# Kernel tuning notes

Measured on AMD Instinct MI355X. Metric: run time of the kernel, lower is better.

The kernel has to match this reference:

```python
import jax, jax.numpy as jnp
import numpy as np

BS, NA = 32, 128
NE = NA * (NA - 1)            # fully-connected directed, no self loops
NU, D = 4, 8                  # num_user, per-user feature dim
FEAT = NU * D                 # 32: node / edge feature dim
CC = 8                        # conv1 out channels (1x1 conv, in_channels=2)
CONV_OUT = CC * NU * D        # 256
EMB = 64                      # embedding size (x_last / output dim)
H1 = 256                      # MLP hidden
MLP1_IN = CONV_OUT + EMB      # layer_idx > 1: concat local_state_j
MLP2_IN = FEAT + EMB + EMB    # x0, x_last, agg_in


def make_edges():
    src, dst = np.meshgrid(np.arange(NA), np.arange(NA), indexing='ij')
    m = src != dst
    return jnp.asarray(np.stack([src[m], dst[m]], axis=1), dtype=jnp.int32)


def setup_inputs() -> dict:
    key = jax.random.key(0)
    ks = jax.random.split(key, 9)
    return {
        "x0": jax.random.normal(ks[0], (BS, NA, FEAT), jnp.float32),
        "x_last": jax.random.normal(ks[1], (BS, NA, EMB), jnp.float32),
        "edge_attr": jax.random.normal(ks[2], (BS, NE, FEAT), jnp.float32),
        "conv_w": jax.random.normal(ks[3], (CC, 2), jnp.float32) * 0.3,
        "conv_b": jnp.zeros((CC,), jnp.float32),
        "mlp1_w1": jax.random.normal(ks[4], (MLP1_IN, H1), jnp.float32) * 0.05,
        "mlp1_b1": jnp.zeros((H1,), jnp.float32),
        "mlp1_w2": jax.random.normal(ks[5], (H1, EMB), jnp.float32) * 0.05,
        "mlp1_b2": jnp.zeros((EMB,), jnp.float32),
        "mlp2_w1": jax.random.normal(ks[6], (MLP2_IN, H1), jnp.float32) * 0.05,
        "mlp2_b1": jnp.zeros((H1,), jnp.float32),
        "mlp2_w2": jax.random.normal(ks[7], (H1, EMB), jnp.float32) * 0.05,
        "mlp2_b2": jnp.zeros((EMB,), jnp.float32),
        "edge_idx": make_edges(),
    }


def reference(x0, x_last, edge_attr, conv_w, conv_b,
              mlp1_w1, mlp1_b1, mlp1_w2, mlp1_b2,
              mlp2_w1, mlp2_b1, mlp2_w2, mlp2_b2, edge_idx):
    src, dst = edge_idx[:, 0], edge_idx[:, 1]
    # --- propagate / local_embedding ---
    nf_j = x0[:, src, :]                 # [B, E, FEAT] gather source node feats
    ls_j = x_last[:, src, :]             # [B, E, EMB]  (layer_idx > 1)
    # torch: cat(node_feat, edge_attr) on user dim then view [N,2,NU,D]
    x = jnp.stack([nf_j.reshape(BS, NE, NU, D),
                   edge_attr.reshape(BS, NE, NU, D)], axis=2)  # [B,E,2,NU,D]
    # 1x1 Conv2d(2 -> CC) + ReLU
    y = jax.nn.relu(jnp.einsum('becud,oc->beoud', x, conv_w)
                    + conv_b[None, None, :, None, None])
    y = y.reshape(BS, NE, CONV_OUT)
    lf = jnp.concatenate([y, ls_j], axis=-1)                   # [B,E,MLP1_IN]
    h = jax.nn.relu(lf @ mlp1_w1 + mlp1_b1)
    local_embed = h @ mlp1_w2 + mlp1_b2                        # [B,E,EMB]
    # per-node segment sum over destination (replaces python loop over agents)
    agg_in = jnp.zeros((BS, NA, EMB), local_embed.dtype).at[:, dst, :].add(local_embed)
    # --- update_embedding ---
    agg = jnp.concatenate([x0, x_last, agg_in], axis=-1)       # [B,NA,MLP2_IN]
    h2 = jax.nn.relu(agg @ mlp2_w1 + mlp2_b1)
    return h2 @ mlp2_w2 + mlp2_b2                              # [B,NA,EMB]
```

## Files before the change

kernel.cpp:

```cpp
#include <hip/hip_runtime.h>
#include <hip/hip_bf16.h>

#define BSg   32
#define NAg   128
#define NEg   16256
#define EMBg  64
#define H1g   256

typedef __attribute__((ext_vector_type(8))) short  short8;
typedef __attribute__((ext_vector_type(4))) float  f32x4;

__device__ __forceinline__ unsigned short f2bf16u(float x) {
    union { __hip_bfloat16 h; unsigned short u; } cv;
    cv.h = __float2bfloat16(x);
    return cv.u;
}
__device__ __forceinline__ unsigned int pack2(float a, float b) {
    union { __hip_bfloat162 h; unsigned int u; } cv;
    cv.h = __float22bfloat162_rn(make_float2(a, b));
    return cv.u;
}

__global__ void pack_weights(const float* __restrict__ w1, unsigned short* __restrict__ w1p)
{
    int i = blockIdx.x * 256 + threadIdx.x;
    if (i < 320 * 256) {
        int k = i >> 8, n = i & 255;
        w1p[(k >> 3) * (256 * 8) + n * 8 + (k & 7)] = f2bf16u(w1[i]);
    }
}

__global__ __launch_bounds__(256, 4) void edge_kernel(
    const float* __restrict__ x0, const float* __restrict__ x_last,
    const float* __restrict__ edge_attr, const float* __restrict__ conv_w,
    const float* __restrict__ conv_b, const unsigned short* __restrict__ w1p,
    const float* __restrict__ b1, const float* __restrict__ w2f,
    const float* __restrict__ b2, float* __restrict__ agg)
{
    __shared__ unsigned short fragA[10 * 4 * 64 * 8];

    const int wgid = (blockIdx.x & 7) * 1024 + (blockIdx.x >> 3);
    const int half = wgid & 1;
    const int bd   = wgid >> 1;
    const int b    = bd >> 7, d = bd & 127;

    const int tid  = threadIdx.x;
    const int wq   = tid >> 6, lane = tid & 63;
    const int llo  = lane & 15, lhi = lane >> 4;
    const int colbase = wq * 64;

    short8 bf0[4];
    #pragma unroll
    for (int n = 0; n < 4; ++n)
        bf0[n] = *(const short8*)&w1p[(lhi * H1g + colbase + n * 16 + llo) * 8];

    {
        const int j  = wq * 16 + llo;
        const int el = half * 64 + j;
        int s = el + (el >= d ? 1 : 0);
        if (s > 127) s = 127;
        int e = s * 127 + d - (s < d ? 1 : 0);
        if (e > NEg - 1) e = NEg - 1;

        const float4* nfp = (const float4*)(x0        + (((size_t)b * NAg + s) << 5) + (lhi << 3));
        const float4* eap = (const float4*)(edge_attr + (((size_t)b * NEg + e) << 5) + (lhi << 3));
        float4 nf0 = nfp[0], nf1 = nfp[1];
        float4 ea0 = eap[0], ea1 = eap[1];

        #pragma unroll
        for (int o = 0; o < 8; ++o) {
            const float w0 = conv_w[2 * o], w1v = conv_w[2 * o + 1], cb = conv_b[o];
            float y0 = fmaxf(fmaf(w0, nf0.x, fmaf(w1v, ea0.x, cb)), 0.f);
            float y1 = fmaxf(fmaf(w0, nf0.y, fmaf(w1v, ea0.y, cb)), 0.f);
            float y2 = fmaxf(fmaf(w0, nf0.z, fmaf(w1v, ea0.z, cb)), 0.f);
            float y3 = fmaxf(fmaf(w0, nf0.w, fmaf(w1v, ea0.w, cb)), 0.f);
            float y4 = fmaxf(fmaf(w0, nf1.x, fmaf(w1v, ea1.x, cb)), 0.f);
            float y5 = fmaxf(fmaf(w0, nf1.y, fmaf(w1v, ea1.y, cb)), 0.f);
            float y6 = fmaxf(fmaf(w0, nf1.z, fmaf(w1v, ea1.z, cb)), 0.f);
            float y7 = fmaxf(fmaf(w0, nf1.w, fmaf(w1v, ea1.w, cb)), 0.f);
            uint4 pk;
            pk.x = pack2(y0, y1); pk.y = pack2(y2, y3);
            pk.z = pack2(y4, y5); pk.w = pack2(y6, y7);
            *(uint4*)&fragA[(((o * 4 + wq) * 64) + lane) * 8] = pk;
        }
        {
            const float4* lsp = (const float4*)(x_last + (((size_t)b * NAg + s) << 6) + (lhi << 4));
            float4 l0 = lsp[0], l1 = lsp[1], l2 = lsp[2], l3 = lsp[3];
            uint4 pa, pb;
            pa.x = pack2(l0.x, l0.y); pa.y = pack2(l0.z, l0.w);
            pa.z = pack2(l1.x, l1.y); pa.w = pack2(l1.z, l1.w);
            pb.x = pack2(l2.x, l2.y); pb.y = pack2(l2.z, l2.w);
            pb.z = pack2(l3.x, l3.y); pb.w = pack2(l3.z, l3.w);
            const int ks8  = 8 + (lhi >> 1);
            const int slot = (ks8 * 4 + wq) * 64 + ((lhi & 1) * 2) * 16 + llo;
            *(uint4*)&fragA[slot * 8]        = pa;
            *(uint4*)&fragA[(slot + 16) * 8] = pb;
        }
    }
    __syncthreads();

    f32x4 acc[4][4];
    #pragma unroll
    for (int m = 0; m < 4; ++m)
        #pragma unroll
        for (int n = 0; n < 4; ++n)
            acc[m][n] = (f32x4){0.f, 0.f, 0.f, 0.f};

    #pragma unroll
    for (int ks = 0; ks < 10; ++ks) {
        short8 af[4], bf[4];
        #pragma unroll
        for (int m = 0; m < 4; ++m)
            af[m] = *(const short8*)&fragA[((ks * 4 + m) * 64 + lane) * 8];
        #pragma unroll
        for (int n = 0; n < 4; ++n) {
            if (ks == 0) bf[n] = bf0[n];
            else         bf[n] = *(const short8*)&w1p[((ks * 4 + lhi) * H1g + colbase + n * 16 + llo) * 8];
        }
        #pragma unroll
        for (int m = 0; m < 4; ++m)
            #pragma unroll
            for (int n = 0; n < 4; ++n)
                acc[m][n] = __builtin_amdgcn_mfma_f32_16x16x32_bf16(af[m], bf[n], acc[m][n], 0, 0, 0);
    }

    float h1s[4];
    {
        float bias1[4];
        #pragma unroll
        for (int n = 0; n < 4; ++n) bias1[n] = b1[colbase + n * 16 + llo];
        #pragma unroll
        for (int n = 0; n < 4; ++n) {
            float p = 0.f;
            #pragma unroll
            for (int m = 0; m < 4; ++m)
                #pragma unroll
                for (int i = 0; i < 4; ++i) {
                    float v = fmaxf(acc[m][n][i] + bias1[n], 0.f);
                    if (!(m == 3 && i == 3 && half == 1 && lhi == 3)) p += v;
                }
            p += __shfl_xor(p, 16, 64);
            p += __shfl_xor(p, 32, 64);
            h1s[n] = p;
        }
    }
    __syncthreads();

    float* h1part = (float*)fragA;
    float* redS   = h1part + 256;

    if (lhi == 0) {
        #pragma unroll
        for (int n = 0; n < 4; ++n) h1part[colbase + n * 16 + llo] = h1s[n];
    }
    __syncthreads();

    {
        const int c = tid & 63, kq = tid >> 6;
        float p = 0.f;
        #pragma unroll 8
        for (int k0 = 0; k0 < 64; ++k0) {
            int k = kq * 64 + k0;
            p = fmaf(h1part[k], w2f[k * 64 + c], p);
        }
        redS[kq * 64 + c] = p;
    }
    __syncthreads();
    if (tid < 64) {
        float v = redS[tid] + redS[64 + tid] + redS[128 + tid] + redS[192 + tid];
        if (half == 0) v += 127.f * b2[tid];
        atomicAdd(&agg[((size_t)bd << 6) + tid], v);
    }
}

__global__ __launch_bounds__(256) void node_kernel(
    const float* __restrict__ x0, const float* __restrict__ x_last,
    const float* __restrict__ agg, const float* __restrict__ w1,
    const float* __restrict__ b1, const float* __restrict__ w2,
    const float* __restrict__ b2, float* __restrict__ out)
{
    __shared__ float lf[8][160];
    __shared__ float h2s[8][257];
    const int tid = threadIdx.x;
    const int r0  = blockIdx.x * 8;

    for (int idx = tid; idx < 8 * 160; idx += 256) {
        int r = idx / 160, c = idx % 160;
        int gr = r0 + r;
        int bb = gr >> 7, a = gr & 127;
        float v;
        if (c < 32)      v = x0[(((size_t)bb * NAg + a) << 5) + c];
        else if (c < 96) v = x_last[(((size_t)bb * NAg + a) << 6) + (c - 32)];
        else             v = agg[((size_t)gr << 6) + (c - 96)];
        lf[r][c] = v;
    }
    __syncthreads();

    {
        const int c = tid;
        float acc[8];
        const float bb = b1[c];
        #pragma unroll
        for (int r = 0; r < 8; ++r) acc[r] = bb;
        for (int k = 0; k < 160; ++k) {
            float wv = w1[k * 256 + c];
            #pragma unroll
            for (int r = 0; r < 8; ++r) acc[r] = fmaf(lf[r][k], wv, acc[r]);
        }
        #pragma unroll
        for (int r = 0; r < 8; ++r) h2s[r][c] = fmaxf(acc[r], 0.f);
    }
    __syncthreads();

    {
        const int n = tid & 63, rq = tid >> 6;
        float acc[2];
        const float bb = b2[n];
        #pragma unroll
        for (int j = 0; j < 2; ++j) acc[j] = bb;
        for (int k = 0; k < 256; ++k) {
            float wv = w2[k * 64 + n];
            #pragma unroll
            for (int j = 0; j < 2; ++j) acc[j] = fmaf(h2s[rq * 2 + j][k], wv, acc[j]);
        }
        #pragma unroll
        for (int j = 0; j < 2; ++j)
            out[((size_t)(r0 + rq * 2 + j) << 6) + n] = acc[j];
    }
}

extern "C" void kernel_launch(void* const* d_in, const int* in_sizes, int n_in,
                              void* d_out, int out_size, void* d_ws, size_t ws_size,
                              hipStream_t stream)
{
    const float* x0       = (const float*)d_in[0];
    const float* x_last   = (const float*)d_in[1];
    const float* edge_attr= (const float*)d_in[2];
    const float* conv_w   = (const float*)d_in[3];
    const float* conv_b   = (const float*)d_in[4];
    const float* mlp1_w1  = (const float*)d_in[5];
    const float* mlp1_b1  = (const float*)d_in[6];
    const float* mlp1_w2  = (const float*)d_in[7];
    const float* mlp1_b2  = (const float*)d_in[8];
    const float* mlp2_w1  = (const float*)d_in[9];
    const float* mlp2_b1  = (const float*)d_in[10];
    const float* mlp2_w2  = (const float*)d_in[11];
    const float* mlp2_b2  = (const float*)d_in[12];

    char* ws = (char*)d_ws;
    float* agg          = (float*)ws;
    unsigned short* w1p = (unsigned short*)(ws + (1 << 20));

    hipMemsetAsync(agg, 0, (size_t)BSg * NAg * EMBg * sizeof(float), stream);
    pack_weights<<<320, 256, 0, stream>>>(mlp1_w1, w1p);
    edge_kernel<<<BSg * NAg * 2, 256, 0, stream>>>(x0, x_last, edge_attr, conv_w, conv_b,
                                                   w1p, mlp1_b1, mlp1_w2, mlp1_b2, agg);
    node_kernel<<<(BSg * NAg) / 8, 256, 0, stream>>>(x0, x_last, agg, mlp2_w1, mlp2_b1,
                                                     mlp2_w2, mlp2_b2, (float*)d_out);
}
```

Measured before the change: 144.3 us.

## Move second MLP GEMM out of edge kernel into separate per-node kernel

The edge kernel now writes its per-half summed hidden activations to a workspace buffer. The second linear layer is applied once per node in a new gemm2 kernel, which adds the two halves and the bias term. This removes the per-block shared-memory GEMV, three barriers and the atomicAdds, and drops the memset of agg. The cost is an extra kernel launch and a global round trip of about 8 MB of hidden activations.

```diff
diff --git a/kernel.cpp b/kernel.cpp
--- a/kernel.cpp
+++ b/kernel.cpp
@@ -34,8 +34,7 @@
     const float* __restrict__ x0, const float* __restrict__ x_last,
     const float* __restrict__ edge_attr, const float* __restrict__ conv_w,
     const float* __restrict__ conv_b, const unsigned short* __restrict__ w1p,
-    const float* __restrict__ b1, const float* __restrict__ w2f,
-    const float* __restrict__ b2, float* __restrict__ agg)
+    const float* __restrict__ b1, float* __restrict__ h1half)
 {
     __shared__ unsigned short fragA[10 * 4 * 64 * 8];
 
@@ -144,33 +143,28 @@
             h1s[n] = p;
         }
     }
-    __syncthreads();
-
-    float* h1part = (float*)fragA;
-    float* redS   = h1part + 256;
-
-    if (lhi == 0) {
-        #pragma unroll
-        for (int n = 0; n < 4; ++n) h1part[colbase + n * 16 + llo] = h1s[n];
-    }
-    __syncthreads();
-
-    {
-        const int c = tid & 63, kq = tid >> 6;
-        float p = 0.f;
-        #pragma unroll 8
-        for (int k0 = 0; k0 < 64; ++k0) {
-            int k = kq * 64 + k0;
-            p = fmaf(h1part[k], w2f[k * 64 + c], p);
-        }
-        redS[kq * 64 + c] = p;
-    }
-    __syncthreads();
-    if (tid < 64) {
-        float v = redS[tid] + redS[64 + tid] + redS[128 + tid] + redS[192 + tid];
-        if (half == 0) v += 127.f * b2[tid];
-        atomicAdd(&agg[((size_t)bd << 6) + tid], v);
-    }
+
+    {
+        float v = h1s[0];
+        if (lhi == 1) v = h1s[1];
+        if (lhi == 2) v = h1s[2];
+        if (lhi == 3) v = h1s[3];
+        h1half[((size_t)wgid << 8) + colbase + lane] = v;
+    }
+}
+
+__global__ __launch_bounds__(256) void gemm2_kernel(
+    const float* __restrict__ h1half, const float* __restrict__ w2f,
+    const float* __restrict__ b2, float* __restrict__ agg)
+{
+    const int r = blockIdx.x * 4 + (threadIdx.x >> 6);
+    const int c = threadIdx.x & 63;
+    const float* h0 = h1half + ((size_t)r << 9);
+    float acc = 127.f * b2[c];
+    #pragma unroll 4
+    for (int k = 0; k < 256; ++k)
+        acc = fmaf(h0[k] + h0[256 + k], w2f[k * 64 + c], acc);
+    agg[((size_t)r << 6) + c] = acc;
 }
 
 __global__ __launch_bounds__(256) void node_kernel(
@@ -250,11 +244,12 @@
     char* ws = (char*)d_ws;
     float* agg          = (float*)ws;
     unsigned short* w1p = (unsigned short*)(ws + (1 << 20));
-
-    hipMemsetAsync(agg, 0, (size_t)BSg * NAg * EMBg * sizeof(float), stream);
+    float* h1half       = (float*)(ws + (2 << 20));
+
     pack_weights<<<320, 256, 0, stream>>>(mlp1_w1, w1p);
     edge_kernel<<<BSg * NAg * 2, 256, 0, stream>>>(x0, x_last, edge_attr, conv_w, conv_b,
-                                                   w1p, mlp1_b1, mlp1_w2, mlp1_b2, agg);
+                                                   w1p, mlp1_b1, h1half);
+    gemm2_kernel<<<1024, 256, 0, stream>>>(h1half, mlp1_w2, mlp1_b2, agg);
     node_kernel<<<(BSg * NAg) / 8, 256, 0, stream>>>(x0, x_last, agg, mlp2_w1, mlp2_b1,
                                                      mlp2_w2, mlp2_b2, (float*)d_out);
 }
```

After: 148.4 us. +2.9%, slower.

## Process both edge halves per workgroup, drop atomics and memset, shrink node tiles

Applied to the files above, without the earlier changes.

Each edge workgroup now loops over both 64-edge halves of a destination node and accumulates the hidden-layer sums in registers. This halves the grid, removes the memset and the atomic adds, and runs the second-layer reduction once per node instead of twice. The node kernel now handles 4 rows per block instead of 8, which doubles its block count and adds unroll hints. The tradeoff is less parallelism in the edge kernel and a serialized loop with extra barriers.

```diff
diff --git a/kernel.cpp b/kernel.cpp
--- a/kernel.cpp
+++ b/kernel.cpp
@@ -39,10 +39,8 @@
 {
     __shared__ unsigned short fragA[10 * 4 * 64 * 8];
 
-    const int wgid = (blockIdx.x & 7) * 1024 + (blockIdx.x >> 3);
-    const int half = wgid & 1;
-    const int bd   = wgid >> 1;
-    const int b    = bd >> 7, d = bd & 127;
+    const int bd = (blockIdx.x & 7) * 512 + (blockIdx.x >> 3);
+    const int b  = bd >> 7, d = bd & 127;
 
     const int tid  = threadIdx.x;
     const int wq   = tid >> 6, lane = tid & 63;
@@ -54,97 +52,101 @@
     for (int n = 0; n < 4; ++n)
         bf0[n] = *(const short8*)&w1p[(lhi * H1g + colbase + n * 16 + llo) * 8];
 
-    {
-        const int j  = wq * 16 + llo;
-        const int el = half * 64 + j;
-        int s = el + (el >= d ? 1 : 0);
-        if (s > 127) s = 127;
-        int e = s * 127 + d - (s < d ? 1 : 0);
-        if (e > NEg - 1) e = NEg - 1;
-
-        const float4* nfp = (const float4*)(x0        + (((size_t)b * NAg + s) << 5) + (lhi << 3));
-        const float4* eap = (const float4*)(edge_attr + (((size_t)b * NEg + e) << 5) + (lhi << 3));
-        float4 nf0 = nfp[0], nf1 = nfp[1];
-        float4 ea0 = eap[0], ea1 = eap[1];
-
-        #pragma unroll
-        for (int o = 0; o < 8; ++o) {
-            const float w0 = conv_w[2 * o], w1v = conv_w[2 * o + 1], cb = conv_b[o];
-            float y0 = fmaxf(fmaf(w0, nf0.x, fmaf(w1v, ea0.x, cb)), 0.f);
-            float y1 = fmaxf(fmaf(w0, nf0.y, fmaf(w1v, ea0.y, cb)), 0.f);
-            float y2 = fmaxf(fmaf(w0, nf0.z, fmaf(w1v, ea0.z, cb)), 0.f);
-            float y3 = fmaxf(fmaf(w0, nf0.w, fmaf(w1v, ea0.w, cb)), 0.f);
-            float y4 = fmaxf(fmaf(w0, nf1.x, fmaf(w1v, ea1.x, cb)), 0.f);
-            float y5 = fmaxf(fmaf(w0, nf1.y, fmaf(w1v, ea1.y, cb)), 0.f);
-            float y6 = fmaxf(fmaf(w0, nf1.z, fmaf(w1v, ea1.z, cb)), 0.f);
-            float y7 = fmaxf(fmaf(w0, nf1.w, fmaf(w1v, ea1.w, cb)), 0.f);
-            uint4 pk;
-            pk.x = pack2(y0, y1); pk.y = pack2(y2, y3);
-            pk.z = pack2(y4, y5); pk.w = pack2(y6, y7);
-            *(uint4*)&fragA[(((o * 4 + wq) * 64) + lane) * 8] = pk;
-        }
+    float h1s[4] = {0.f, 0.f, 0.f, 0.f};
+
+    #pragma unroll 1
+    for (int t = 0; t < 2; ++t) {
         {
-            const float4* lsp = (const float4*)(x_last + (((size_t)b * NAg + s) << 6) + (lhi << 4));
-            float4 l0 = lsp[0], l1 = lsp[1], l2 = lsp[2], l3 = lsp[3];
-            uint4 pa, pb;
-            pa.x = pack2(l0.x, l0.y); pa.y = pack2(l0.z, l0.w);
-            pa.z = pack2(l1.x, l1.y); pa.w = pack2(l1.z, l1.w);
-            pb.x = pack2(l2.x, l2.y); pb.y = pack2(l2.z, l2.w);
-            pb.z = pack2(l3.x, l3.y); pb.w = pack2(l3.z, l3.w);
-            const int ks8  = 8 + (lhi >> 1);
-            const int slot = (ks8 * 4 + wq) * 64 + ((lhi & 1) * 2) * 16 + llo;
-            *(uint4*)&fragA[slot * 8]        = pa;
-            *(uint4*)&fragA[(slot + 16) * 8] = pb;
-        }
-    }
-    __syncthreads();
-
-    f32x4 acc[4][4];
-    #pragma unroll
-    for (int m = 0; m < 4; ++m)
-        #pragma unroll
-        for (int n = 0; n < 4; ++n)
-            acc[m][n] = (f32x4){0.f, 0.f, 0.f, 0.f};
-
-    #pragma unroll
-    for (int ks = 0; ks < 10; ++ks) {
-        short8 af[4], bf[4];
+            const int j  = wq * 16 + llo;
+            const int el = t * 64 + j;
+            int s = el + (el >= d ? 1 : 0);
+            if (s > 127) s = 127;
+            int e = s * 127 + d - (s < d ? 1 : 0);
+            if (e > NEg - 1) e = NEg - 1;
+
+            const float4* nfp = (const float4*)(x0        + (((size_t)b * NAg + s) << 5) + (lhi << 3));
+            const float4* eap = (const float4*)(edge_attr + (((size_t)b * NEg + e) << 5) + (lhi << 3));
+            float4 nf0 = nfp[0], nf1 = nfp[1];
+            float4 ea0 = eap[0], ea1 = eap[1];
+
+            #pragma unroll
+            for (int o = 0; o < 8; ++o) {
+                const float w0 = conv_w[2 * o], w1v = conv_w[2 * o + 1], cb = conv_b[o];
+                float y0 = fmaxf(fmaf(w0, nf0.x, fmaf(w1v, ea0.x, cb)), 0.f);
+                float y1 = fmaxf(fmaf(w0, nf0.y, fmaf(w1v, ea0.y, cb)), 0.f);
+                float y2 = fmaxf(fmaf(w0, nf0.z, fmaf(w1v, ea0.z, cb)), 0.f);
+                float y3 = fmaxf(fmaf(w0, nf0.w, fmaf(w1v, ea0.w, cb)), 0.f);
+                float y4 = fmaxf(fmaf(w0, nf1.x, fmaf(w1v, ea1.x, cb)), 0.f);
+                float y5 = fmaxf(fmaf(w0, nf1.y, fmaf(w1v, ea1.y, cb)), 0.f);
+                float y6 = fmaxf(fmaf(w0, nf1.z, fmaf(w1v, ea1.z, cb)), 0.f);
+                float y7 = fmaxf(fmaf(w0, nf1.w, fmaf(w1v, ea1.w, cb)), 0.f);
+                uint4 pk;
+                pk.x = pack2(y0, y1); pk.y = pack2(y2, y3);
+                pk.z = pack2(y4, y5); pk.w = pack2(y6, y7);
+                *(uint4*)&fragA[(((o * 4 + wq) * 64) + lane) * 8] = pk;
+            }
+            {
+                const float4* lsp = (const float4*)(x_last + (((size_t)b * NAg + s) << 6) + (lhi << 4));
+                float4 l0 = lsp[0], l1 = lsp[1], l2 = lsp[2], l3 = lsp[3];
+                uint4 pa, pb;
+                pa.x = pack2(l0.x, l0.y); pa.y = pack2(l0.z, l0.w);
+                pa.z = pack2(l1.x, l1.y); pa.w = pack2(l1.z, l1.w);
+                pb.x = pack2(l2.x, l2.y); pb.y = pack2(l2.z, l2.w);
+                pb.z = pack2(l3.x, l3.y); pb.w = pack2(l3.z, l3.w);
+                const int ks8  = 8 + (lhi >> 1);
+                const int slot = (ks8 * 4 + wq) * 64 + ((lhi & 1) * 2) * 16 + llo;
+                *(uint4*)&fragA[slot * 8]        = pa;
+                *(uint4*)&fragA[(slot + 16) * 8] = pb;
+            }
+        }
+        __syncthreads();
+
+        f32x4 acc[4][4];
         #pragma unroll
         for (int m = 0; m < 4; ++m)
-            af[m] = *(const short8*)&fragA[((ks * 4 + m) * 64 + lane) * 8];
-        #pragma unroll
-        for (int n = 0; n < 4; ++n) {
-            if (ks == 0) bf[n] = bf0[n];
-            else         bf[n] = *(const short8*)&w1p[((ks * 4 + lhi) * H1g + colbase + n * 16 + llo) * 8];
-        }
-        #pragma unroll
-        for (int m = 0; m < 4; ++m)
             #pragma unroll
             for (int n = 0; n < 4; ++n)
-                acc[m][n] = __builtin_amdgcn_mfma_f32_16x16x32_bf16(af[m], bf[n], acc[m][n], 0, 0, 0);
-    }
-
-    float h1s[4];
-    {
-        float bias1[4];
-        #pragma unroll
-        for (int n = 0; n < 4; ++n) bias1[n] = b1[colbase + n * 16 + llo];
-        #pragma unroll
-        for (int n = 0; n < 4; ++n) {
-            float p = 0.f;
+                acc[m][n] = (f32x4){0.f, 0.f, 0.f, 0.f};
+
+        #pragma unroll
+        for (int ks = 0; ks < 10; ++ks) {
+            short8 af[4], bf[4];
+            #pragma unroll
+            for (int m = 0; m < 4; ++m)
+                af[m] = *(const short8*)&fragA[((ks * 4 + m) * 64 + lane) * 8];
+            #pragma unroll
+            for (int n = 0; n < 4; ++n) {
+                if (ks == 0) bf[n] = bf0[n];
+                else         bf[n] = *(const short8*)&w1p[((ks * 4 + lhi) * H1g + colbase + n * 16 + llo) * 8];
+            }
             #pragma unroll
             for (int m = 0; m < 4; ++m)
                 #pragma unroll
-                for (int i = 0; i < 4; ++i) {
-                    float v = fmaxf(acc[m][n][i] + bias1[n], 0.f);
-                    if (!(m == 3 && i == 3 && half == 1 && lhi == 3)) p += v;
-                }
-            p += __shfl_xor(p, 16, 64);
-            p += __shfl_xor(p, 32, 64);
-            h1s[n] = p;
-        }
-    }
-    __syncthreads();
+                for (int n = 0; n < 4; ++n)
+                    acc[m][n] = __builtin_amdgcn_mfma_f32_16x16x32_bf16(af[m], bf[n], acc[m][n], 0, 0, 0);
+        }
+
+        {
+            float bias1[4];
+            #pragma unroll
+            for (int n = 0; n < 4; ++n) bias1[n] = b1[colbase + n * 16 + llo];
+            #pragma unroll
+            for (int n = 0; n < 4; ++n) {
+                float p = 0.f;
+                #pragma unroll
+                for (int m = 0; m < 4; ++m)
+                    #pragma unroll
+                    for (int i = 0; i < 4; ++i) {
+                        float v = fmaxf(acc[m][n][i] + bias1[n], 0.f);
+                        if (!(m == 3 && i == 3 && t == 1 && lhi == 3)) p += v;
+                    }
+                p += __shfl_xor(p, 16, 64);
+                p += __shfl_xor(p, 32, 64);
+                h1s[n] += p;
+            }
+        }
+        __syncthreads();
+    }
 
     float* h1part = (float*)fragA;
     float* redS   = h1part + 256;
@@ -167,9 +169,9 @@
     }
     __syncthreads();
     if (tid < 64) {
-        float v = redS[tid] + redS[64 + tid] + redS[128 + tid] + redS[192 + tid];
-        if (half == 0) v += 127.f * b2[tid];
-        atomicAdd(&agg[((size_t)bd << 6) + tid], v);
+        float v = redS[tid] + redS[64 + tid] + redS[128 + tid] + redS[192 + tid]
+                + 127.f * b2[tid];
+        agg[((size_t)bd << 6) + tid] = v;
     }
 }
 
@@ -179,12 +181,12 @@
     const float* __restrict__ b1, const float* __restrict__ w2,
     const float* __restrict__ b2, float* __restrict__ out)
 {
-    __shared__ float lf[8][160];
-    __shared__ float h2s[8][257];
+    __shared__ float lf[4][160];
+    __shared__ float h2s[4][257];
     const int tid = threadIdx.x;
-    const int r0  = blockIdx.x * 8;
-
-    for (int idx = tid; idx < 8 * 160; idx += 256) {
+    const int r0  = blockIdx.x * 4;
+
+    for (int idx = tid; idx < 4 * 160; idx += 256) {
         int r = idx / 160, c = idx % 160;
         int gr = r0 + r;
         int bb = gr >> 7, a = gr & 127;
@@ -198,34 +200,28 @@
 
     {
         const int c = tid;
-        float acc[8];
+        float acc[4];
         const float bb = b1[c];
         #pragma unroll
-        for (int r = 0; r < 8; ++r) acc[r] = bb;
+        for (int r = 0; r < 4; ++r) acc[r] = bb;
+        #pragma unroll 4
         for (int k = 0; k < 160; ++k) {
             float wv = w1[k * 256 + c];
             #pragma unroll
-            for (int r = 0; r < 8; ++r) acc[r] = fmaf(lf[r][k], wv, acc[r]);
-        }
-        #pragma unroll
-        for (int r = 0; r < 8; ++r) h2s[r][c] = fmaxf(acc[r], 0.f);
+            for (int r = 0; r < 4; ++r) acc[r] = fmaf(lf[r][k], wv, acc[r]);
+        }
+        #pragma unroll
+        for (int r = 0; r < 4; ++r) h2s[r][c] = fmaxf(acc[r], 0.f);
     }
     __syncthreads();
 
     {
         const int n = tid & 63, rq = tid >> 6;
-        float acc[2];
-        const float bb = b2[n];
-        #pragma unroll
-        for (int j = 0; j < 2; ++j) acc[j] = bb;
-        for (int k = 0; k < 256; ++k) {
-            float wv = w2[k * 64 + n];
-            #pragma unroll
-            for (int j = 0; j < 2; ++j) acc[j] = fmaf(h2s[rq * 2 + j][k], wv, acc[j]);
-        }
-        #pragma unroll
-        for (int j = 0; j < 2; ++j)
-            out[((size_t)(r0 + rq * 2 + j) << 6) + n] = acc[j];
+        float acc = b2[n];
+        #pragma unroll 4
+        for (int k = 0; k < 256; ++k)
+            acc = fmaf(h2s[rq][k], w2[k * 64 + n], acc);
+        out[((size_t)(r0 + rq) << 6) + n] = acc;
     }
 }
 
@@ -248,13 +244,12 @@
     const float* mlp2_b2  = (const float*)d_in[12];
 
     char* ws = (char*)d_ws;
-    float* agg          = (float*)ws;
-    unsigned short* w1p = (unsigned short*)(ws + (1 << 20));
-
-    hipMemsetAsync(agg, 0, (size_t)BSg * NAg * EMBg * sizeof(float), stream);
+    unsigned short* w1p = (unsigned short*)ws;
+    float* agg          = (float*)(ws + (1 << 20));
+
     pack_weights<<<320, 256, 0, stream>>>(mlp1_w1, w1p);
-    edge_kernel<<<BSg * NAg * 2, 256, 0, stream>>>(x0, x_last, edge_attr, conv_w, conv_b,
-                                                   w1p, mlp1_b1, mlp1_w2, mlp1_b2, agg);
-    node_kernel<<<(BSg * NAg) / 8, 256, 0, stream>>>(x0, x_last, agg, mlp2_w1, mlp2_b1,
+    edge_kernel<<<BSg * NAg, 256, 0, stream>>>(x0, x_last, edge_attr, conv_w, conv_b,
+                                               w1p, mlp1_b1, mlp1_w2, mlp1_b2, agg);
+    node_kernel<<<(BSg * NAg) / 4, 256, 0, stream>>>(x0, x_last, agg, mlp2_w1, mlp2_b1,
                                                      mlp2_w2, mlp2_b2, (float*)d_out);
 }
```

Result: slower. 337.6 us (+134.0%).
